# Optimization experiments

Hardware: AMD Instinct MI355X
Metric: run time of the kernel (lower is better)

Reference implementation:

```python
import jax, jax.numpy as jnp
import numpy as np

NEG_SLOPE = 0.2
N, IN_DIM, OUT_DIM, N_HEADS = 4096, 512, 512, 4
D_K = OUT_DIM // N_HEADS


def setup_inputs() -> dict:
    key = jax.random.key(0)
    k1, k2, k3, k4, k5 = jax.random.split(key, 5)
    H = jax.random.normal(k1, (N, IN_DIM), dtype=jnp.float32)
    A = jax.random.randint(k2, (N, N), 0, 2, dtype=jnp.int32)
    W = jax.random.normal(k3, (IN_DIM, OUT_DIM), dtype=jnp.float32) * (1.0 / np.sqrt(IN_DIM))
    a_l = jax.random.normal(k4, (N_HEADS, D_K), dtype=jnp.float32) * 0.1
    a_r = jax.random.normal(k5, (N_HEADS, D_K), dtype=jnp.float32) * 0.1
    return {"H": H, "A": A, "W": W, "a_l": a_l, "a_r": a_r}


def reference(H, A, W, a_l, a_r):
    n = H.shape[0]
    # mask = (A + I) > 0, shape (N, N); self-loops always allowed
    mask = (A + jnp.eye(n, dtype=A.dtype)) > 0
    # Wh: (N, heads, d_k)
    Wh = (H @ W).reshape(n, N_HEADS, D_K)
    sl = jnp.einsum('nhd,hd->nh', Wh, a_l)  # (N, heads)
    sr = jnp.einsum('nhd,hd->nh', Wh, a_r)  # (N, heads)
    # e[i, h, j] = leaky_relu(sl[i,h] + sr[j,h])
    e = jax.nn.leaky_relu(sl[:, :, None] + sr.T[None, :, :], negative_slope=NEG_SLOPE)
    e = jnp.where(mask[:, None, :], e, -jnp.inf)
    alpha = jnp.nan_to_num(jax.nn.softmax(e, axis=2), nan=0.0)  # dropout is identity at eval
    # out[i, h, :] = sum_j alpha[i,h,j] * Wh[j,h,:]
    out = jnp.einsum('nhm,mhd->nhd', alpha, Wh).reshape(n, OUT_DIM)
    return jax.nn.elu(out)
```

## Files before the change

kernel.cpp:

```cpp
#include <hip/hip_runtime.h>

typedef unsigned short ushort_t;
typedef __attribute__((ext_vector_type(8)))  short  short8;
typedef __attribute__((ext_vector_type(4)))  short  short4v;
typedef __attribute__((ext_vector_type(4)))  float  float4v;
typedef __attribute__((ext_vector_type(4)))  int    int4v;

#define N_NODES 4096
#define NHEADS  4
#define DK      128
#define ODIM    512
#define KDIM    512

__device__ __forceinline__ float bf2f(ushort_t u) {
    return __uint_as_float(((unsigned)u) << 16);
}
__device__ __forceinline__ ushort_t f2bf_rne(float f) {
    unsigned u = __float_as_uint(f);
    u += 0x7fffu + ((u >> 16) & 1u);
    return (ushort_t)(u >> 16);
}

__global__ __launch_bounds__(256) void pack_mask_k(const int* __restrict__ A,
                                                   unsigned long long* __restrict__ P,
                                                   const ushort_t* __restrict__ Hraw,
                                                   int* __restrict__ flag,
                                                   const void* __restrict__ W,
                                                   ushort_t* __restrict__ WT,
                                                   float* __restrict__ sl,
                                                   float* __restrict__ sr)
{
    __shared__ ushort_t lt[64][72];
    __shared__ int dcnt[4];
    const int tid = threadIdx.x;
    const int bx  = blockIdx.x;

    if (bx == 0 && tid < 64) {
        const int lane = tid;
        int cnt = 0;
        #pragma unroll
        for (int s = 0; s < 16; ++s) {
            ushort_t v = Hraw[(lane * 16 + s) * 2];
            int e = (v >> 7) & 0xFF;
            cnt += (((e >= 90) && (e <= 140)) || (v == 0)) ? 1 : 0;
        }
        #pragma unroll
        for (int off = 32; off; off >>= 1) cnt += __shfl_down(cnt, off);
        if (lane == 0) *flag = (cnt < 768) ? 1 : 0;
    }

    {
        const int lane = tid & 63;
        #pragma unroll
        for (int kk = 0; kk < 4; ++kk) {
            const int flat4 = (bx * 4 + kk) * 256 + tid;
            const int row   = flat4 >> 10;
            const int col0  = (flat4 << 2) & 4095;
            const int4v a   = ((const int4v*)A)[flat4];
            unsigned nib = 0;
            #pragma unroll
            for (int j = 0; j < 4; ++j)
                nib |= ((a[j] != 0) || (row == col0 + j)) ? (1u << j) : 0u;
            unsigned long long v = (unsigned long long)nib << ((lane & 15) * 4);
            v |= __shfl_xor(v, 1);
            v |= __shfl_xor(v, 2);
            v |= __shfl_xor(v, 4);
            v |= __shfl_xor(v, 8);
            if ((lane & 15) == 0) P[flat4 >> 4] = v;
        }
    }

    if (bx >= 64 && bx < 96) {
        const int idx = (bx - 64) * 256 + tid;
        float4v z;
        #pragma unroll
        for (int e = 0; e < 4; ++e) z[e] = 0.f;
        if (idx < 4096) ((float4v*)sl)[idx] = z;
        else            ((float4v*)sr)[idx - 4096] = z;
    }

    if (bx < 64) {
        int cnt = 0;
        #pragma unroll
        for (int s = 0; s < 4; ++s) {
            ushort_t v = Hraw[(tid * 4 + s) * 2];
            int e = (v >> 7) & 0xFF;
            cnt += (((e >= 90) && (e <= 140)) || (v == 0)) ? 1 : 0;
        }
        #pragma unroll
        for (int off = 32; off; off >>= 1) cnt += __shfl_down(cnt, off);
        if ((tid & 63) == 0) dcnt[tid >> 6] = cnt;
        __syncthreads();
        const int f32 = (dcnt[0] + dcnt[1] + dcnt[2] + dcnt[3]) < 768;

        const int ti = bx >> 3, tj = bx & 7;
        const int r = tid >> 2, c2 = tid & 3;
        const size_t eo = (size_t)(ti * 64 + r) * KDIM + tj * 64 + c2 * 16;
        if (f32) {
            const float4v* src = (const float4v*)((const float*)W + eo);
            float4v f0 = src[0], f1 = src[1], f2 = src[2], f3 = src[3];
            #pragma unroll
            for (int e = 0; e < 4; ++e) {
                lt[r][c2 * 16 +  0 + e] = f2bf_rne(f0[e]);
                lt[r][c2 * 16 +  4 + e] = f2bf_rne(f1[e]);
                lt[r][c2 * 16 +  8 + e] = f2bf_rne(f2[e]);
                lt[r][c2 * 16 + 12 + e] = f2bf_rne(f3[e]);
            }
        } else {
            const short8* src = (const short8*)((const ushort_t*)W + eo);
            short8 v0 = src[0];
            short8 v1 = src[1];
            *(short8*)&lt[r][c2 * 16]     = v0;
            *(short8*)&lt[r][c2 * 16 + 8] = v1;
        }
        __syncthreads();
        #pragma unroll
        for (int itr = 0; itr < 2; ++itr) {
            int idx = itr * 256 + tid;
            int n = idx >> 3, c = idx & 7;
            short8 vv;
            #pragma unroll
            for (int e = 0; e < 8; ++e) vv[e] = (short)lt[c * 8 + e][n];
            *(short8*)(WT + (size_t)(tj * 64 + n) * KDIM + ti * 64 + c * 8) = vv;
        }
    }
}

__global__ __launch_bounds__(256) void gemm_wht_dual_k(const void* __restrict__ H,
                                                       const ushort_t* __restrict__ WT,
                                                       ushort_t* __restrict__ WhT,
                                                       const int* __restrict__ flag,
                                                       const void* __restrict__ al,
                                                       const void* __restrict__ ar,
                                                       float* __restrict__ sl,
                                                       float* __restrict__ sr)
{
    __shared__ ushort_t Bs[64 * KDIM];
    __shared__ ushort_t lt[64][72];
    const int f32 = *flag;
    const int tid  = threadIdx.x;
    const int lane = tid & 63;
    const int wid  = tid >> 6;
    const int quad = lane >> 4;
    const int l15  = lane & 15;
    const int bm = blockIdx.x & 63, bn = blockIdx.x >> 6;
    const int i0 = bm * 64, n0 = bn * 64;

    #pragma unroll
    for (int rr = 0; rr < 16; ++rr) {
        const int n = wid * 16 + rr;
        const ushort_t* src = WT + (size_t)(n0 + n) * KDIM + (size_t)((lane ^ (n & 3)) * 8);
        __builtin_amdgcn_global_load_lds(
            (const __attribute__((address_space(1))) void*)src,
            (__attribute__((address_space(3))) void*)(Bs + n * KDIM), 16, 0, 0);
    }
    asm volatile("s_waitcnt vmcnt(0)" ::: "memory");
    __syncthreads();

    const size_t aoff = (size_t)(i0 + wid * 16 + l15) * KDIM + quad * 8;

    float4v acc0, acc1, acc2, acc3;
    #pragma unroll
    for (int e = 0; e < 4; ++e) { acc0[e] = 0.f; acc1[e] = 0.f; acc2[e] = 0.f; acc3[e] = 0.f; }

    const int sx = l15 & 3;

    #pragma unroll 4
    for (int k8 = 0; k8 < 64; k8 += 4) {
        short8 a;
        if (f32) {
            const float4v* fp = (const float4v*)((const float*)H + aoff + (size_t)k8 * 8);
            float4v x0 = fp[0], x1 = fp[1];
            #pragma unroll
            for (int e = 0; e < 4; ++e) {
                a[e]     = (short)f2bf_rne(x0[e]);
                a[4 + e] = (short)f2bf_rne(x1[e]);
            }
        } else {
            a = *(const short8*)((const ushort_t*)H + aoff + (size_t)k8 * 8);
        }
        const int s = (quad + k8) ^ sx;
        short8 b0 = *(const short8*)(Bs + ( 0 + l15) * KDIM + s * 8);
        short8 b1 = *(const short8*)(Bs + (16 + l15) * KDIM + s * 8);
        short8 b2 = *(const short8*)(Bs + (32 + l15) * KDIM + s * 8);
        short8 b3 = *(const short8*)(Bs + (48 + l15) * KDIM + s * 8);
        acc0 = __builtin_amdgcn_mfma_f32_16x16x32_bf16(a, b0, acc0, 0, 0, 0);
        acc1 = __builtin_amdgcn_mfma_f32_16x16x32_bf16(a, b1, acc1, 0, 0, 0);
        acc2 = __builtin_amdgcn_mfma_f32_16x16x32_bf16(a, b2, acc2, 0, 0, 0);
        acc3 = __builtin_amdgcn_mfma_f32_16x16x32_bf16(a, b3, acc3, 0, 0, 0);
    }

    #pragma unroll
    for (int r = 0; r < 4; ++r) {
        int m = wid * 16 + quad * 4 + r;
        lt[ 0 + l15][m] = f2bf_rne(acc0[r]);
        lt[16 + l15][m] = f2bf_rne(acc1[r]);
        lt[32 + l15][m] = f2bf_rne(acc2[r]);
        lt[48 + l15][m] = f2bf_rne(acc3[r]);
    }
    __syncthreads();
    #pragma unroll
    for (int itr = 0; itr < 2; ++itr) {
        int idx = itr * 256 + tid;
        int n = idx >> 3, c = idx & 7;
        short8 v = *(const short8*)&lt[n][c * 8];
        *(short8*)(WhT + (size_t)(n0 + n) * N_NODES + i0 + c * 8) = v;
    }

    {
        const int h2 = n0 >> 7;
        const int d0 = n0 & 127;
        const int m  = tid >> 2;
        const int part = tid & 3;
        float psl = 0.f, psr = 0.f;
        #pragma unroll
        for (int k = 0; k < 16; ++k) {
            int n = part * 16 + k;
            float wv = bf2f(lt[n][m]);
            float av = f32 ? ((const float*)al)[h2 * DK + d0 + n]
                           : bf2f(((const ushort_t*)al)[h2 * DK + d0 + n]);
            float bv = f32 ? ((const float*)ar)[h2 * DK + d0 + n]
                           : bf2f(((const ushort_t*)ar)[h2 * DK + d0 + n]);
            psl += wv * av;
            psr += wv * bv;
        }
        psl += __shfl_down(psl, 2); psl += __shfl_down(psl, 1);
        psr += __shfl_down(psr, 2); psr += __shfl_down(psr, 1);
        if (part == 0) {
            atomicAdd(&sl[h2 * N_NODES + i0 + m], psl);
            atomicAdd(&sr[h2 * N_NODES + i0 + m], psr);
        }
    }
}

__global__ __launch_bounds__(1024, 4) void attn_full_k(const ushort_t* __restrict__ WhT,
                                                       const unsigned* __restrict__ Apack,
                                                       const float* __restrict__ sl,
                                                       const float* __restrict__ sr,
                                                       void* __restrict__ out,
                                                       const int* __restrict__ flag)
{
    __shared__ char smem[147456] __attribute__((aligned(16)));
    ushort_t* vbuf = (ushort_t*)smem;
    unsigned (*mbuf)[128] = (unsigned (*)[128])(smem + 98304);
    float*    srs  = (float*)(smem + 131072);

    const int f32  = *flag;
    const int tid  = threadIdx.x;
    const int lane = tid & 63;
    const int wid  = tid >> 6;
    const int wq   = wid & 3;
    const int js   = wid >> 2;
    const int quad = lane >> 4;
    const int l15  = lane & 15;
    const int bx   = blockIdx.x;
    const int h    = bx & 3;
    const int i0   = (bx >> 2) << 6;

    const float C1 = 1.44269504f;

    for (int j = tid; j < 4096; j += 1024) srs[j] = sr[h * N_NODES + j] * C1;
    for (int t = tid; t < 64 * 128; t += 1024) {
        int r = t >> 7, c = t & 127;
        mbuf[r][c ^ (r & 31)] = Apack[(size_t)(i0 + r) * 128 + c];
    }
    const int myrow = wq * 16 + l15;
    const float slv = sl[h * N_NODES + i0 + myrow] * C1;
    __syncthreads();

    float4v acc[8];
    #pragma unroll
    for (int nt = 0; nt < 8; ++nt)
        #pragma unroll
        for (int e = 0; e < 4; ++e) acc[nt][e] = 0.f;
    float4v accden;
    #pragma unroll
    for (int e = 0; e < 4; ++e) accden[e] = 0.f;

    short8 ones;
    #pragma unroll
    for (int e = 0; e < 8; ++e) ones[e] = (short)0x3F80;

    const int dl = lane >> 4;
    const int s4 = lane & 15;
    const ushort_t* gq0 = WhT + (size_t)(h * DK + wid * 8 + 0 + dl) * N_NODES
                              + (size_t)((s4 ^ (0 + dl)) * 8);
    const ushort_t* gq1 = WhT + (size_t)(h * DK + wid * 8 + 4 + dl) * N_NODES
                              + (size_t)((s4 ^ (4 + dl)) * 8);

    #define DMA_WIN(BUF, IW)                                                           \
        {   ushort_t* lb_ = vbuf + (BUF) * 16384 + wid * 1024;                         \
            __builtin_amdgcn_global_load_lds(                                          \
                (const __attribute__((address_space(1))) void*)(gq0 + (size_t)(IW) * 128), \
                (__attribute__((address_space(3))) void*)(lb_), 16, 0, 0);             \
            __builtin_amdgcn_global_load_lds(                                          \
                (const __attribute__((address_space(1))) void*)(gq1 + (size_t)(IW) * 128), \
                (__attribute__((address_space(3))) void*)(lb_ + 512), 16, 0, 0);       \
        }

    DMA_WIN(0, 0)
    DMA_WIN(1, 1)

    const int rs = ((js * 4 + quad) ^ (l15 & 7)) * 8;

    #pragma unroll 1
    for (int iw = 0; iw < 32; ++iw) {
        const unsigned wa = mbuf[myrow][(iw * 4 + js) ^ (myrow & 31)];
        const float4v s0 = *(const float4v*)&srs[iw * 128 + js * 32 + quad * 8];
        const float4v s1 = *(const float4v*)&srs[iw * 128 + js * 32 + quad * 8 + 4];

        short8 pf;
        #pragma unroll
        for (int jj = 0; jj < 8; ++jj) {
            const int bit = quad * 8 + jj;
            float srj = (jj < 4) ? s0[jj] : s1[jj - 4];
            float x = slv + srj;
            float t = fmaxf(x, x * 0.2f);
            t = ((wa >> bit) & 1u) ? t : -1e30f;
            pf[jj] = (short)(ushort_t)(__float_as_uint(__builtin_amdgcn_exp2f(t)) >> 16);
        }

        if (iw == 31) { asm volatile("s_waitcnt vmcnt(0)" ::: "memory"); }
        else          { asm volatile("s_waitcnt vmcnt(2)" ::: "memory"); }
        asm volatile("s_barrier" ::: "memory");
        if (iw < 30) DMA_WIN((iw + 2) % 3, iw + 2)

        const ushort_t* vB = vbuf + (iw % 3) * 16384;
        #pragma unroll
        for (int nt = 0; nt < 8; ++nt) {
            short8 b = *(const short8*)(vB + (nt * 16 + l15) * 128 + rs);
            acc[nt] = __builtin_amdgcn_mfma_f32_16x16x32_bf16(pf, b, acc[nt], 0, 0, 0);
        }
        accden = __builtin_amdgcn_mfma_f32_16x16x32_bf16(pf, ones, accden, 0, 0, 0);
    }
    #undef DMA_WIN

    float* red  = (float*)smem;
    float* lsum = (float*)(smem + 98304);
    __syncthreads();

    if (js != 0) {
        float* rp = red + (size_t)((js - 1) * 4 + wq) * 2048;
        #pragma unroll
        for (int nt = 0; nt < 8; ++nt)
            #pragma unroll
            for (int r = 0; r < 4; ++r)
                rp[(quad * 4 + r) * 128 + nt * 16 + l15] = acc[nt][r];
        if (l15 == 0) {
            #pragma unroll
            for (int r = 0; r < 4; ++r)
                lsum[js * 64 + wq * 16 + quad * 4 + r] = accden[r];
        }
    }
    __syncthreads();
    if (js == 0) {
        float rinv[4];
        #pragma unroll
        for (int r = 0; r < 4; ++r) {
            const int rowo = wq * 16 + quad * 4 + r;
            float den = accden[r] + lsum[64 + rowo] + lsum[128 + rowo] + lsum[192 + rowo];
            rinv[r] = 1.0f / fmaxf(den, 1e-37f);
        }
        #pragma unroll
        for (int nt = 0; nt < 8; ++nt)
            #pragma unroll
            for (int r = 0; r < 4; ++r) {
                const int ri = (quad * 4 + r) * 128 + nt * 16 + l15;
                float v = (acc[nt][r]
                           + red[(size_t)(0 * 4 + wq) * 2048 + ri]
                           + red[(size_t)(1 * 4 + wq) * 2048 + ri]
                           + red[(size_t)(2 * 4 + wq) * 2048 + ri]) * rinv[r];
                float e = __builtin_amdgcn_exp2f(v * C1) - 1.0f;
                float o = (v > 0.f) ? v : e;
                const size_t oidx = (size_t)(i0 + wq * 16 + quad * 4 + r) * ODIM
                                  + h * DK + nt * 16 + l15;
                if (f32) ((float*)out)[oidx] = o;
                else     ((ushort_t*)out)[oidx] = f2bf_rne(o);
            }
    }
}

extern "C" void kernel_launch(void* const* d_in, const int* in_sizes, int n_in,
                              void* d_out, int out_size, void* d_ws, size_t ws_size,
                              hipStream_t stream)
{
    const void* H  = d_in[0];
    const int*  A  = (const int*)d_in[1];
    const void* W  = d_in[2];
    const void* al = d_in[3];
    const void* ar = d_in[4];

    if (ws_size < (7u << 20)) return;

    char* ws = (char*)d_ws;
    ushort_t* WhT   = (ushort_t*)ws;
    unsigned long long* Apack = (unsigned long long*)(ws + (4u << 20));
    ushort_t* WT    = (ushort_t*)(ws + (6u << 20));
    float*    sl    = (float*)(ws + (6u << 20) + (512u << 10));
    float*    sr    = (float*)(ws + (6u << 20) + (576u << 10));
    int*      flag  = (int*)(ws + (6u << 20) + (640u << 10));

    pack_mask_k    <<<4096,  256, 0, stream>>>(A, Apack, (const ushort_t*)H, flag,
                                               W, WT, sl, sr);
    gemm_wht_dual_k<<<512,   256, 0, stream>>>(H, WT, WhT, flag, al, ar, sl, sr);
    attn_full_k    <<<256,  1024, 0, stream>>>(WhT, (const unsigned*)Apack, sl, sr,
                                               (void*)d_out, flag);
}
```

Before: 159.6 us.

## Double-buffer 256-column Wh windows and read mask bits directly from global

The attention loop now handles 256-column windows in 16 iterations with double buffering, replacing 128-column windows over 32 iterations with triple buffering. Each wave issues two MFMAs per output tile per window, and the DMA uses a new XOR swizzle. The staged LDS copy of the packed mask is removed; each thread prefetches its mask words straight from global one window ahead. Wave priority is raised around the MFMA block, and a plain __syncthreads replaces the vmcnt-based waits. The aim is fewer barriers and a smaller prologue, at the cost of a shallower prefetch pipeline and per-iteration global mask loads.

```diff
diff --git a/kernel.cpp b/kernel.cpp
--- a/kernel.cpp
+++ b/kernel.cpp
@@ -242,7 +242,6 @@
 {
     __shared__ char smem[147456] __attribute__((aligned(16)));
     ushort_t* vbuf = (ushort_t*)smem;
-    unsigned (*mbuf)[128] = (unsigned (*)[128])(smem + 98304);
     float*    srs  = (float*)(smem + 131072);
 
     const int f32  = *flag;
@@ -260,12 +259,9 @@
     const float C1 = 1.44269504f;
 
     for (int j = tid; j < 4096; j += 1024) srs[j] = sr[h * N_NODES + j] * C1;
-    for (int t = tid; t < 64 * 128; t += 1024) {
-        int r = t >> 7, c = t & 127;
-        mbuf[r][c ^ (r & 31)] = Apack[(size_t)(i0 + r) * 128 + c];
-    }
     const int myrow = wq * 16 + l15;
     const float slv = sl[h * N_NODES + i0 + myrow] * C1;
+    const unsigned* mrow = Apack + (size_t)(i0 + myrow) * 128;
     __syncthreads();
 
     float4v acc[8];
@@ -281,57 +277,75 @@
     #pragma unroll
     for (int e = 0; e < 8; ++e) ones[e] = (short)0x3F80;
 
-    const int dl = lane >> 4;
-    const int s4 = lane & 15;
-    const ushort_t* gq0 = WhT + (size_t)(h * DK + wid * 8 + 0 + dl) * N_NODES
-                              + (size_t)((s4 ^ (0 + dl)) * 8);
-    const ushort_t* gq1 = WhT + (size_t)(h * DK + wid * 8 + 4 + dl) * N_NODES
-                              + (size_t)((s4 ^ (4 + dl)) * 8);
-
-    #define DMA_WIN(BUF, IW)                                                           \
-        {   ushort_t* lb_ = vbuf + (BUF) * 16384 + wid * 1024;                         \
+    const int rrow  = lane >> 5;
+    const int s32   = lane & 31;
+    const int dbase = wid * 8;
+
+    #define DMA_WIN(BUF, W)                                                            \
+        { _Pragma("unroll")                                                            \
+          for (int q_ = 0; q_ < 4; ++q_) {                                             \
+            const int d_  = dbase + q_ * 2 + rrow;                                     \
+            const int ch_ = s32 ^ (d_ & 31);                                           \
+            const ushort_t* g_ = WhT + (size_t)(h * DK + d_) * N_NODES                 \
+                                      + (size_t)(W) * 256 + (size_t)ch_ * 8;           \
             __builtin_amdgcn_global_load_lds(                                          \
-                (const __attribute__((address_space(1))) void*)(gq0 + (size_t)(IW) * 128), \
-                (__attribute__((address_space(3))) void*)(lb_), 16, 0, 0);             \
-            __builtin_amdgcn_global_load_lds(                                          \
-                (const __attribute__((address_space(1))) void*)(gq1 + (size_t)(IW) * 128), \
-                (__attribute__((address_space(3))) void*)(lb_ + 512), 16, 0, 0);       \
-        }
-
+                (const __attribute__((address_space(1))) void*)g_,                     \
+                (__attribute__((address_space(3))) void*)(vbuf + (BUF) * 32768         \
+                                                         + wid * 2048 + q_ * 512),     \
+                16, 0, 0);                                                             \
+          } }
+
+    unsigned wa0 = mrow[js * 2 + 0];
+    unsigned wa1 = mrow[js * 2 + 1];
     DMA_WIN(0, 0)
-    DMA_WIN(1, 1)
-
-    const int rs = ((js * 4 + quad) ^ (l15 & 7)) * 8;
 
     #pragma unroll 1
-    for (int iw = 0; iw < 32; ++iw) {
-        const unsigned wa = mbuf[myrow][(iw * 4 + js) ^ (myrow & 31)];
-        const float4v s0 = *(const float4v*)&srs[iw * 128 + js * 32 + quad * 8];
-        const float4v s1 = *(const float4v*)&srs[iw * 128 + js * 32 + quad * 8 + 4];
-
-        short8 pf;
+    for (int w = 0; w < 16; ++w) {
+        __syncthreads();
+        unsigned wa0n = wa0, wa1n = wa1;
+        if (w < 15) {
+            wa0n = mrow[(w + 1) * 8 + js * 2 + 0];
+            wa1n = mrow[(w + 1) * 8 + js * 2 + 1];
+            DMA_WIN((w + 1) & 1, w + 1)
+        }
+
+        const float4v a0 = *(const float4v*)&srs[w * 256 + js * 64 + quad * 8];
+        const float4v a1 = *(const float4v*)&srs[w * 256 + js * 64 + quad * 8 + 4];
+        const float4v b0 = *(const float4v*)&srs[w * 256 + js * 64 + 32 + quad * 8];
+        const float4v b1 = *(const float4v*)&srs[w * 256 + js * 64 + 32 + quad * 8 + 4];
+
+        short8 pf0, pf1;
         #pragma unroll
         for (int jj = 0; jj < 8; ++jj) {
             const int bit = quad * 8 + jj;
-            float srj = (jj < 4) ? s0[jj] : s1[jj - 4];
-            float x = slv + srj;
+            float x = slv + ((jj < 4) ? a0[jj] : a1[jj - 4]);
             float t = fmaxf(x, x * 0.2f);
-            t = ((wa >> bit) & 1u) ? t : -1e30f;
-            pf[jj] = (short)(ushort_t)(__float_as_uint(__builtin_amdgcn_exp2f(t)) >> 16);
-        }
-
-        if (iw == 31) { asm volatile("s_waitcnt vmcnt(0)" ::: "memory"); }
-        else          { asm volatile("s_waitcnt vmcnt(2)" ::: "memory"); }
-        asm volatile("s_barrier" ::: "memory");
-        if (iw < 30) DMA_WIN((iw + 2) % 3, iw + 2)
-
-        const ushort_t* vB = vbuf + (iw % 3) * 16384;
+            t = ((wa0 >> bit) & 1u) ? t : -1e30f;
+            pf0[jj] = (short)(ushort_t)(__float_as_uint(__builtin_amdgcn_exp2f(t)) >> 16);
+            float y = slv + ((jj < 4) ? b0[jj] : b1[jj - 4]);
+            float u = fmaxf(y, y * 0.2f);
+            u = ((wa1 >> bit) & 1u) ? u : -1e30f;
+            pf1[jj] = (short)(ushort_t)(__float_as_uint(__builtin_amdgcn_exp2f(u)) >> 16);
+        }
+
+        const ushort_t* vB = vbuf + (w & 1) * 32768;
+        __builtin_amdgcn_s_setprio(1);
         #pragma unroll
         for (int nt = 0; nt < 8; ++nt) {
-            short8 b = *(const short8*)(vB + (nt * 16 + l15) * 128 + rs);
-            acc[nt] = __builtin_amdgcn_mfma_f32_16x16x32_bf16(pf, b, acc[nt], 0, 0, 0);
-        }
-        accden = __builtin_amdgcn_mfma_f32_16x16x32_bf16(pf, ones, accden, 0, 0, 0);
+            const int roff  = (nt * 16 + l15) * 256;
+            const int dlow  = (nt & 1) * 16 + l15;
+            const int slot0 = (js * 8 + 0 + quad) ^ dlow;
+            const int slot1 = (js * 8 + 4 + quad) ^ dlow;
+            short8 bv0 = *(const short8*)(vB + roff + slot0 * 8);
+            short8 bv1 = *(const short8*)(vB + roff + slot1 * 8);
+            acc[nt] = __builtin_amdgcn_mfma_f32_16x16x32_bf16(pf0, bv0, acc[nt], 0, 0, 0);
+            acc[nt] = __builtin_amdgcn_mfma_f32_16x16x32_bf16(pf1, bv1, acc[nt], 0, 0, 0);
+        }
+        accden = __builtin_amdgcn_mfma_f32_16x16x32_bf16(pf0, ones, accden, 0, 0, 0);
+        accden = __builtin_amdgcn_mfma_f32_16x16x32_bf16(pf1, ones, accden, 0, 0, 0);
+        __builtin_amdgcn_s_setprio(0);
+
+        wa0 = wa0n; wa1 = wa1n;
     }
     #undef DMA_WIN
 
```

Measured after the change: 158.9 us (median of 2 runs). Within noise of the previous version (-0.4%).
